# Kernel optimization log

Hardware: AMD Instinct MI355X
Metric: run time of the kernel (lower is better)

## Reference

```python
import jax, jax.numpy as jnp
import numpy as np

B, S, H, NH, HD = 2, 2048, 1024, 16, 64
RD = 16            # rotary_dim = head_dim * 0.25
W = 16             # mini_context_length (sliding window)
SCALE = HD ** -0.5
ROPE_BASE = 10000.0


def setup_inputs() -> dict:
    key = jax.random.key(0)
    ks = jax.random.split(key, 10)
    p = lambda k, shape: (jax.random.normal(k, shape, dtype=jnp.float32) * 0.02)
    return {
        "hidden_states": jax.random.normal(ks[0], (B, S, H), dtype=jnp.float32),
        "Wqkv": p(ks[1], (3 * H, H)), "bqkv": p(ks[2], (3 * H,)),
        "Wqa": p(ks[3], (H, H)),      "bqa": p(ks[4], (H,)),
        "Wka": p(ks[5], (H, H)),      "bka": p(ks[6], (H,)),
        "Wd": p(ks[7], (H, H)),       "bd": p(ks[8], (H,)),
    }


def _rotate_half(x):
    x1, x2 = jnp.split(x, 2, axis=-1)
    return jnp.concatenate([-x2, x1], axis=-1)


def _apply_rope(q, k, seq_len):
    # GPT-NeoX style rotary on the first RD dims. q,k: [B,NH,S,RD]
    inv_freq = 1.0 / (ROPE_BASE ** (jnp.arange(0, RD, 2, dtype=jnp.float32) / RD))
    t = jnp.arange(seq_len, dtype=jnp.float32)
    freqs = jnp.outer(t, inv_freq)                     # [S, RD//2]
    emb = jnp.concatenate([freqs, freqs], axis=-1)     # [S, RD]
    cos = jnp.cos(emb)[None, None]                      # [1,1,S,RD]
    sin = jnp.sin(emb)[None, None]
    return q * cos + _rotate_half(q) * sin, k * cos + _rotate_half(k) * sin


def reference(hidden_states, Wqkv, bqkv, Wqa, bqa, Wka, bka, Wd, bd):
    b, s, _ = hidden_states.shape
    qkv = hidden_states @ Wqkv.T + bqkv                       # [B,S,3H]
    qkv = qkv.reshape(b, s, 3, NH, HD).transpose(2, 0, 3, 1, 4)
    q, k, v = qkv[0], qkv[1], qkv[2]                          # [B,NH,S,HD]

    q_rot, k_rot = _apply_rope(q[..., :RD], k[..., :RD], s)
    q = jnp.concatenate([q_rot, q[..., RD:]], axis=-1)
    k = jnp.concatenate([k_rot, k[..., RD:]], axis=-1)

    # ----- Stage 1: sliding-window local attention (vectorized) -----
    pos = jnp.arange(s)
    idx = pos[:, None] - (W - 1) + jnp.arange(W)[None, :]     # [S,W]
    valid = idx >= 0
    idxc = jnp.clip(idx, 0, s - 1)
    k_win = k[:, :, idxc, :]                                   # [B,NH,S,W,HD]
    v_win = v[:, :, idxc, :]
    scores = jnp.einsum('bhsd,bhswd->bhsw', q, k_win) * SCALE
    scores = jnp.where(valid[None, None], scores, -jnp.inf)
    probs = jax.nn.softmax(scores, axis=-1)
    A = jnp.einsum('bhsw,bhswd->bhsd', probs, v_win)           # [B,NH,S,HD]

    A_hidden = A.transpose(0, 2, 1, 3).reshape(b, s, H)        # [B,S,H]

    # ----- Stage 2: causal global attention over A -----
    qa = (A_hidden @ Wqa.T + bqa).reshape(b, s, NH, HD).transpose(0, 2, 1, 3)
    ka = (A_hidden @ Wka.T + bka).reshape(b, s, NH, HD).transpose(0, 2, 1, 3)
    g = jnp.einsum('bhqd,bhkd->bhqk', qa, ka) * SCALE          # [B,NH,S,S]
    causal = pos[:, None] >= pos[None, :]
    g = jnp.where(causal[None, None], g, -jnp.inf)
    pg = jax.nn.softmax(g, axis=-1)
    out = jnp.einsum('bhqk,bhkd->bhqd', pg, A)                 # [B,NH,S,HD]
    out = out.transpose(0, 2, 1, 3).reshape(b, s, H)
    return out @ Wd.T + bd
```

## Files before the change

### kernel.cpp

```cpp
#include <hip/hip_runtime.h>
#include <hip/hip_bf16.h>
#include <cstdint>
#include <cstddef>

typedef __bf16 bf16;
typedef __bf16 bf16x2 __attribute__((ext_vector_type(2)));
typedef __bf16 bf16x4 __attribute__((ext_vector_type(4)));
typedef __bf16 bf16x8 __attribute__((ext_vector_type(8)));
typedef float  f32x4  __attribute__((ext_vector_type(4)));
typedef int    i32x4  __attribute__((ext_vector_type(4)));

#define DEVINL __device__ __forceinline__

constexpr int   Bc  = 2, Sc = 2048, Hc = 1024, NHc = 16, HDc = 64;
constexpr int   Tc  = Bc * Sc;
constexpr float L2E = 1.44269504088896340736f;
constexpr float NEG_BIG = -1.0e30f;

typedef __attribute__((address_space(1))) void AS1void;
typedef __attribute__((address_space(3))) void AS3void;

DEVINL void load_lds16(const bf16* g, bf16* l) {
  __builtin_amdgcn_global_load_lds((AS1void*)g, (AS3void*)l, 16, 0, 0);
}

DEVINL int packbf(float a, float b) {
  union { bf16x2 h; int i; } u;
  u.h[0] = (bf16)a; u.h[1] = (bf16)b;
  return u.i;
}


__global__ __launch_bounds__(256)
void convert_all(const float* __restrict__ hs, const float* __restrict__ Wqkv,
                 const float* __restrict__ Wqa, const float* __restrict__ Wka,
                 const float* __restrict__ Wd, const float* __restrict__ bqa,
                 const float* __restrict__ bka,
                 bf16* __restrict__ hsb, bf16* __restrict__ wqkvb,
                 bf16* __restrict__ wqakab, bf16* __restrict__ wdb,
                 float* __restrict__ bqaka) {
  const int blk = blockIdx.x;
  if (blk >= 5120) {
    const int i = threadIdx.x * 8;
    const float* src = (i < 1024) ? (bqa + i) : (bka + i - 1024);
    *(f32x4*)(bqaka + i)     = *(const f32x4*)src;
    *(f32x4*)(bqaka + i + 4) = *(const f32x4*)(src + 4);
    return;
  }
  const float* src; bf16* dst; int base;
  if      (blk < 2048) { src = hs;   dst = hsb;                    base = blk; }
  else if (blk < 3584) { src = Wqkv; dst = wqkvb;                  base = blk - 2048; }
  else if (blk < 4096) { src = Wqa;  dst = wqakab;                 base = blk - 3584; }
  else if (blk < 4608) { src = Wka;  dst = wqakab + 1024 * 1024;   base = blk - 4096; }
  else                 { src = Wd;   dst = wdb;                    base = blk - 4608; }
  const int i = (base * 256 + threadIdx.x) * 8;
  f32x4 a = *(const f32x4*)(src + i);
  f32x4 b = *(const f32x4*)(src + i + 4);
  bf16x8 v;
#pragma unroll
  for (int j = 0; j < 4; j++) { v[j] = (bf16)a[j]; v[4 + j] = (bf16)b[j]; }
  *(bf16x8*)(dst + i) = v;
}

template <typename CT>
__global__ __launch_bounds__(256, 3)
void gemm128(const bf16* __restrict__ A, const bf16* __restrict__ Bw,
             const float* __restrict__ bias, CT* __restrict__ C,
             int M, int N, int K) {
  __shared__ __attribute__((aligned(16))) bf16 As[128 * 64];
  __shared__ __attribute__((aligned(16))) bf16 Bs[128 * 64];

  const int tid = threadIdx.x, wv = tid >> 6, lane = tid & 63;
  const int m0 = blockIdx.y * 128, n0 = blockIdx.x * 128;
  const int col = lane & 15, quad = lane >> 4;
  const int wrow = (wv >> 1) * 64, wcol = (wv & 1) * 64;

  f32x4 acc[4][4];
#pragma unroll
  for (int i = 0; i < 4; i++)
#pragma unroll
    for (int j = 0; j < 4; j++) acc[i][j] = f32x4{0.f, 0.f, 0.f, 0.f};

  const int srow = tid >> 3;
  const int scol = (((tid & 7) ^ (srow & 7)) << 3);
  const bf16* Ag = A  + (size_t)(m0 + srow) * K + scol;
  const bf16* Bg = Bw + (size_t)(n0 + srow) * K + scol;
  const int cs = col & 7;

  for (int k0 = 0; k0 < K; k0 += 64) {
#pragma unroll
    for (int c = 0; c < 4; c++) {
      load_lds16(Ag + (size_t)(c * 32) * K + k0, As + c * 2048 + tid * 8);
      load_lds16(Bg + (size_t)(c * 32) * K + k0, Bs + c * 2048 + tid * 8);
    }
    __syncthreads();
#pragma unroll
    for (int kk = 0; kk < 64; kk += 32) {
      const int so = ((((kk >> 3) + quad) ^ cs) << 3);
      bf16x8 af[4], bfr[4];
#pragma unroll
      for (int i = 0; i < 4; i++)
        af[i] = *(const bf16x8*)(As + (wrow + i * 16 + col) * 64 + so);
#pragma unroll
      for (int j = 0; j < 4; j++)
        bfr[j] = *(const bf16x8*)(Bs + (wcol + j * 16 + col) * 64 + so);
#pragma unroll
      for (int i = 0; i < 4; i++)
#pragma unroll
        for (int j = 0; j < 4; j++)
          acc[i][j] = __builtin_amdgcn_mfma_f32_16x16x32_bf16(af[i], bfr[j], acc[i][j], 0, 0, 0);
    }
    __syncthreads();
  }

#pragma unroll
  for (int j = 0; j < 4; j++) {
    const int c = n0 + wcol + j * 16 + col;
    const float bv = bias[c];
#pragma unroll
    for (int i = 0; i < 4; i++)
#pragma unroll
      for (int r = 0; r < 4; r++) {
        const int rr = m0 + wrow + i * 16 + quad * 4 + r;
        C[(size_t)rr * N + c] = (CT)(acc[i][j][r] + bv);
      }
  }
}

template <typename CT>
__global__ __launch_bounds__(256, 4)
void gemm6464(const bf16* __restrict__ A, const bf16* __restrict__ Bw,
              const float* __restrict__ bias, CT* __restrict__ C,
              int M, int N, int K) {
  __shared__ __attribute__((aligned(16))) bf16 As[64 * 64];
  __shared__ __attribute__((aligned(16))) bf16 Bs[64 * 64];

  const int tid = threadIdx.x, wv = tid >> 6, lane = tid & 63;
  const int m0 = blockIdx.y * 64, n0 = blockIdx.x * 64;
  const int col = lane & 15, quad = lane >> 4;

  f32x4 acc[4];
#pragma unroll
  for (int j = 0; j < 4; j++) acc[j] = f32x4{0.f, 0.f, 0.f, 0.f};

  const int srow = tid >> 3;
  const int scol = (((tid & 7) ^ (srow & 7)) << 3);
  const bf16* Ag = A  + (size_t)(m0 + srow) * K + scol;
  const bf16* Bg = Bw + (size_t)(n0 + srow) * K + scol;
  const int cs = col & 7;

  for (int k0 = 0; k0 < K; k0 += 64) {
#pragma unroll
    for (int c = 0; c < 2; c++) {
      load_lds16(Ag + (size_t)(c * 32) * K + k0, As + c * 2048 + tid * 8);
      load_lds16(Bg + (size_t)(c * 32) * K + k0, Bs + c * 2048 + tid * 8);
    }
    __syncthreads();
#pragma unroll
    for (int kk = 0; kk < 64; kk += 32) {
      const int so = ((((kk >> 3) + quad) ^ cs) << 3);
      bf16x8 af = *(const bf16x8*)(As + (wv * 16 + col) * 64 + so);
#pragma unroll
      for (int j = 0; j < 4; j++) {
        bf16x8 bfr = *(const bf16x8*)(Bs + (j * 16 + col) * 64 + so);
        acc[j] = __builtin_amdgcn_mfma_f32_16x16x32_bf16(af, bfr, acc[j], 0, 0, 0);
      }
    }
    __syncthreads();
  }

#pragma unroll
  for (int j = 0; j < 4; j++) {
    const int c = n0 + j * 16 + col;
    const float bv = bias[c];
#pragma unroll
    for (int r = 0; r < 4; r++) {
      const int rr = m0 + wv * 16 + quad * 4 + r;
      C[(size_t)rr * N + c] = (CT)(acc[j][r] + bv);
    }
  }
}

__global__ __launch_bounds__(256)
void window_attn(const bf16* __restrict__ qkv, bf16* __restrict__ Ah,
                 bf16* __restrict__ VTg) {
  __shared__ __attribute__((aligned(16))) bf16 Kw[31 * 72];
  __shared__ __attribute__((aligned(16))) bf16 Vw[31 * 72];
  const int g  = blockIdx.x;
  const int st = g & 127;
  const int h  = (g >> 7) & 15;
  const int b  = g >> 11;
  const int s0 = st * 16;
  const int tid = threadIdx.x;

  if ((tid < 124) || (tid >= 128 && tid < 252)) {
    const bool isK = tid < 124;
    const int lt  = isK ? tid : tid - 128;
    const int r   = lt >> 2, off = (lt & 3) << 4;
    int sidx = s0 - 15 + r; if (sidx < 0) sidx = 0;
    const bf16* src = qkv + (size_t)(b * Sc + sidx) * 3072 + (isK ? 1024 : 2048) + h * 64 + off;
    bf16x8 v0 = *(const bf16x8*)src;
    bf16x8 v1 = *(const bf16x8*)(src + 8);
    if (isK && off == 0) {
#pragma unroll
      for (int j = 0; j < 8; j++) {
        const float invf = exp2f(-(float)j * 1.66096404744368128f);
        float sn, csn;
        sincosf((float)sidx * invf, &sn, &csn);
        const float x1 = (float)v0[j], x2 = (float)v1[j];
        v0[j] = (bf16)(x1 * csn - x2 * sn);
        v1[j] = (bf16)(x2 * csn + x1 * sn);
      }
    }
    bf16* dst = (isK ? Kw : Vw) + r * 72 + off;
    *(bf16x8*)dst       = v0;
    *(bf16x8*)(dst + 8) = v1;
  }
  __syncthreads();

  const int wv = tid >> 6, lane = tid & 63;
  const int subq = lane >> 4, lane16 = lane & 15;
  const int s = s0 + wv * 4 + subq;
  const int t = b * Sc + s;
  const int d0 = lane16 * 4;

  float qd[4];
  {
    bf16x4 qv = *(const bf16x4*)(qkv + (size_t)t * 3072 + h * 64 + d0);
#pragma unroll
    for (int j = 0; j < 4; j++) qd[j] = (float)qv[j];
  }
  float pd[4];
#pragma unroll
  for (int j = 0; j < 4; j++) pd[j] = __shfl_xor(qd[j], 2, 64);
  if (lane16 < 4) {
#pragma unroll
    for (int j = 0; j < 4; j++) {
      const int jabs = d0 + j;
      const float invf = exp2f(-(float)(jabs & 7) * 1.66096404744368128f);
      float sn, csn;
      sincosf((float)s * invf, &sn, &csn);
      qd[j] = (jabs < 8) ? (qd[j] * csn - pd[j] * sn) : (qd[j] * csn + pd[j] * sn);
    }
  }

  float sc[16];
#pragma unroll
  for (int w = 0; w < 16; w++) {
    const int idxp = s - 15 + w;
    const int row = idxp - s0 + 15;
    bf16x4 kv = *(const bf16x4*)(Kw + row * 72 + d0);
    float p = qd[0] * (float)kv[0] + qd[1] * (float)kv[1] +
              qd[2] * (float)kv[2] + qd[3] * (float)kv[3];
#pragma unroll
    for (int m = 1; m < 16; m <<= 1) p += __shfl_xor(p, m, 64);
    sc[w] = (idxp < 0) ? NEG_BIG : p * 0.125f;
  }
  float mx = sc[0];
#pragma unroll
  for (int w = 1; w < 16; w++) mx = fmaxf(mx, sc[w]);
  float sum = 0.f;
#pragma unroll
  for (int w = 0; w < 16; w++) { sc[w] = exp2f((sc[w] - mx) * L2E); sum += sc[w]; }
  const float inv = 1.0f / fmaxf(sum, 1e-30f);

  float acc[4] = {0.f, 0.f, 0.f, 0.f};
#pragma unroll
  for (int w = 0; w < 16; w++) {
    const int idxp = s - 15 + w;
    const int row = idxp - s0 + 15;
    bf16x4 vv = *(const bf16x4*)(Vw + row * 72 + d0);
#pragma unroll
    for (int j = 0; j < 4; j++) acc[j] += sc[w] * (float)vv[j];
  }
  bf16x4 ov;
#pragma unroll
  for (int j = 0; j < 4; j++) ov[j] = (bf16)(acc[j] * inv);
  *(bf16x4*)(Ah + (size_t)t * 1024 + h * 64 + d0) = ov;
  bf16* vt = VTg + (((size_t)(b * 16 + h)) * 64 + d0) * 2048 + s;
#pragma unroll
  for (int j = 0; j < 4; j++) vt[(size_t)j * 2048] = ov[j];
}

__global__ __launch_bounds__(256, 4)
void flash_attn(const bf16* __restrict__ Q, const bf16* __restrict__ Kt,
                const bf16* __restrict__ VTg, bf16* __restrict__ O) {
  constexpr int QS = 2048;
  constexpr float SHIFT = 16.0f;
  __shared__ __attribute__((aligned(16))) bf16 K_lds[128 * 64];
  __shared__ __attribute__((aligned(16))) bf16 VT_lds[64 * 128];

  const int tid = threadIdx.x, wv = tid >> 6, lane = tid & 63;
  const int bh = blockIdx.x;
  const int y  = blockIdx.y;
  const int gq = y & 7, kq = y >> 3;
  const int qt = (kq == 0) ? gq : (kq == 1) ? (15 - gq)
               : (kq == 2) ? (16 + gq) : (31 - gq);
  const int b = bh >> 4, h = bh & 15;
  const int col = lane & 15, quad = lane >> 4;
  const size_t bS = (size_t)b * Sc;
  const int hd = h * 64;

  const int krow = tid >> 3;
  const int kcol = (((tid & 7) ^ (krow & 7)) << 3);
  const int vrow = tid >> 4;
  const int vcol = (((tid & 15) ^ vrow) << 3);
  const int cs8 = col & 7;

  const int idxA = (col + 16 * ((2 * quad) & 3)) << 2;
  const int idxB = (col + 16 * ((2 * quad + 1) & 3)) << 2;

  const int qbase = qt * 64 + wv * 16;
  const int nkt = (qt + 2) >> 1;

  const bf16* qptr = Q + (bS + qbase + col) * QS + hd + quad * 8;
  bf16x8 qf[2];
  qf[0] = *(const bf16x8*)qptr;
  qf[1] = *(const bf16x8*)(qptr + 32);
#pragma unroll
  for (int hh = 0; hh < 2; hh++)
#pragma unroll
    for (int j = 0; j < 8; j++) qf[hh][j] = (bf16)((float)qf[hh][j] * 0.125f);

  f32x4 oacc[4];
#pragma unroll
  for (int i = 0; i < 4; i++) oacc[i] = f32x4{0.f, 0.f, 0.f, 0.f};
  float lsum = 0.f;

  for (int kt0 = 0; kt0 < nkt; kt0++) {
    const int k0 = kt0 * 128;
#pragma unroll
    for (int c = 0; c < 4; c++) {
      load_lds16(Kt + (bS + k0 + c * 32 + krow) * QS + hd + kcol,
                 K_lds + c * 2048 + tid * 8);
      load_lds16(VTg + ((size_t)bh * 64 + c * 16 + vrow) * 2048 + k0 + vcol,
                 VT_lds + c * 2048 + tid * 8);
    }
    __syncthreads();

    f32x4 sacc[8];
#pragma unroll
    for (int sub = 0; sub < 8; sub++) {
      f32x4 a = f32x4{0.f, 0.f, 0.f, 0.f};
#pragma unroll
      for (int hh = 0; hh < 2; hh++) {
        const int so = (((hh * 4 + quad) ^ cs8) << 3);
        bf16x8 kf = *(const bf16x8*)(K_lds + (sub * 16 + col) * 64 + so);
        a = __builtin_amdgcn_mfma_f32_16x16x32_bf16(kf, qf[hh], a, 0, 0, 0);
      }
      sacc[sub] = a;
    }
    if (kt0 == nkt - 1) {
      const int qq = qbase + col;
#pragma unroll
      for (int sub = 0; sub < 8; sub++)
#pragma unroll
        for (int r = 0; r < 4; r++) {
          const int key = k0 + sub * 16 + quad * 4 + r;
          if (key > qq) sacc[sub][r] = NEG_BIG;
        }
    }
#pragma unroll
    for (int sub = 0; sub < 8; sub++)
#pragma unroll
      for (int r = 0; r < 4; r++)
        sacc[sub][r] = exp2f(sacc[sub][r] * L2E - SHIFT);
#pragma unroll
    for (int sub = 0; sub < 8; sub++)
      lsum += (sacc[sub][0] + sacc[sub][1]) + (sacc[sub][2] + sacc[sub][3]);
    int pkl[8], pkh[8];
#pragma unroll
    for (int sub = 0; sub < 8; sub++) {
      pkl[sub] = packbf(sacc[sub][0], sacc[sub][1]);
      pkh[sub] = packbf(sacc[sub][2], sacc[sub][3]);
    }
#pragma unroll
    for (int c = 0; c < 4; c++) {
      const int sLo = 2 * c, sHi = 2 * c + 1;
      i32x4 w;
      {
        int aL = __builtin_amdgcn_ds_bpermute(idxA, pkl[sLo]);
        int aH = __builtin_amdgcn_ds_bpermute(idxA, pkl[sHi]);
        w[0] = (quad < 2) ? aL : aH;
      }
      {
        int aL = __builtin_amdgcn_ds_bpermute(idxA, pkh[sLo]);
        int aH = __builtin_amdgcn_ds_bpermute(idxA, pkh[sHi]);
        w[1] = (quad < 2) ? aL : aH;
      }
      {
        int aL = __builtin_amdgcn_ds_bpermute(idxB, pkl[sLo]);
        int aH = __builtin_amdgcn_ds_bpermute(idxB, pkl[sHi]);
        w[2] = (quad < 2) ? aL : aH;
      }
      {
        int aL = __builtin_amdgcn_ds_bpermute(idxB, pkh[sLo]);
        int aH = __builtin_amdgcn_ds_bpermute(idxB, pkh[sHi]);
        w[3] = (quad < 2) ? aL : aH;
      }
      union { i32x4 wi; bf16x8 v; } pb;
      pb.wi = w;
      const int vso = (((c * 4 + quad) ^ col) << 3);
#pragma unroll
      for (int nb = 0; nb < 4; nb++) {
        bf16x8 vf = *(const bf16x8*)(VT_lds + (nb * 16 + col) * 128 + vso);
        oacc[nb] = __builtin_amdgcn_mfma_f32_16x16x32_bf16(vf, pb.v, oacc[nb], 0, 0, 0);
      }
    }
    __syncthreads();
  }

  lsum += __shfl_xor(lsum, 16, 64);
  lsum += __shfl_xor(lsum, 32, 64);
  const float inv = 1.0f / fmaxf(lsum, 1e-37f);
  const int qq = qbase + col;
#pragma unroll
  for (int nb = 0; nb < 4; nb++) {
    bf16x4 ov;
#pragma unroll
    for (int r = 0; r < 4; r++) ov[r] = (bf16)(oacc[nb][r] * inv);
    *(bf16x4*)(O + (bS + qq) * 1024 + hd + nb * 16 + quad * 4) = ov;
  }
}

extern "C" void kernel_launch(void* const* d_in, const int* in_sizes, int n_in,
                              void* d_out, int out_size, void* d_ws, size_t ws_size,
                              hipStream_t stream) {
  (void)in_sizes; (void)n_in; (void)out_size; (void)ws_size;
  const float* hs   = (const float*)d_in[0];
  const float* Wqkv = (const float*)d_in[1];
  const float* bqkv = (const float*)d_in[2];
  const float* Wqa  = (const float*)d_in[3];
  const float* bqa  = (const float*)d_in[4];
  const float* Wka  = (const float*)d_in[5];
  const float* bka  = (const float*)d_in[6];
  const float* Wd   = (const float*)d_in[7];
  const float* bd   = (const float*)d_in[8];
  float* out = (float*)d_out;

  const size_t TH = (size_t)Tc * Hc;
  bf16* dob   = (bf16*)d_out;
  bf16* hsb   = dob;
  bf16* wqkvb = dob + TH;
  bf16* Ah    = dob;
  bf16* VTg   = dob + TH;
  bf16* ws     = (bf16*)d_ws;
  bf16* qkv    = ws;
  bf16* qaka   = ws;
  bf16* oh     = ws + 2 * TH;
  bf16* wqakab = ws + 3 * TH;
  bf16* wdb    = wqakab + 2 * 1024 * 1024;
  float* bqaka = (float*)(wdb + 1024 * 1024);

  convert_all<<<dim3(5121), 256, 0, stream>>>(hs, Wqkv, Wqa, Wka, Wd, bqa, bka,
                                              hsb, wqkvb, wqakab, wdb, bqaka);

  gemm128<bf16><<<dim3(24, 32), 256, 0, stream>>>(hsb, wqkvb, bqkv, qkv, Tc, 3 * Hc, Hc);
  window_attn<<<dim3(Tc * NHc / 16), 256, 0, stream>>>(qkv, Ah, VTg);
  gemm128<bf16><<<dim3(16, 32), 256, 0, stream>>>(Ah, wqakab, bqaka, qaka, Tc, 2 * Hc, Hc);
  flash_attn<<<dim3(Bc * NHc, 32), 256, 0, stream>>>(qaka, qaka + Hc, VTg, oh);
  gemm6464<float><<<dim3(16, 64), 256, 0, stream>>>(oh, wdb, bd, out, Tc, Hc, Hc);
}
```

Baseline: 240.8 us.

## Fuse fp32 weight conversion into GEMM B-tile staging

Drops the separate weight-conversion pass. The GEMMs now read fp32 weights directly and convert them to bf16 while staging tiles into LDS, and the Q/K projection weights and biases are selected per row through a split pointer instead of being pre-concatenated. This removes one pass that writes about 12 MB of converted weights and the buffers that held them. In exchange, the B operand is loaded through registers instead of the async global-to-LDS path, at twice the bytes per tile and re-read by every M block, which may slow the GEMM main loops.

```diff
diff --git a/kernel.cpp b/kernel.cpp
--- a/kernel.cpp
+++ b/kernel.cpp
@@ -24,6 +24,16 @@
   __builtin_amdgcn_global_load_lds((AS1void*)g, (AS3void*)l, 16, 0, 0);
 }
 
+DEVINL void stage8(const bf16* g, bf16* l) { load_lds16(g, l); }
+DEVINL void stage8(const float* g, bf16* l) {
+  f32x4 a = *(const f32x4*)g;
+  f32x4 b = *(const f32x4*)(g + 4);
+  bf16x8 v;
+#pragma unroll
+  for (int j = 0; j < 4; j++) { v[j] = (bf16)a[j]; v[4 + j] = (bf16)b[j]; }
+  *(bf16x8*)l = v;
+}
+
 DEVINL int packbf(float a, float b) {
   union { bf16x2 h; int i; } u;
   u.h[0] = (bf16)a; u.h[1] = (bf16)b;
@@ -32,40 +42,21 @@
 
 
 __global__ __launch_bounds__(256)
-void convert_all(const float* __restrict__ hs, const float* __restrict__ Wqkv,
-                 const float* __restrict__ Wqa, const float* __restrict__ Wka,
-                 const float* __restrict__ Wd, const float* __restrict__ bqa,
-                 const float* __restrict__ bka,
-                 bf16* __restrict__ hsb, bf16* __restrict__ wqkvb,
-                 bf16* __restrict__ wqakab, bf16* __restrict__ wdb,
-                 float* __restrict__ bqaka) {
-  const int blk = blockIdx.x;
-  if (blk >= 5120) {
-    const int i = threadIdx.x * 8;
-    const float* src = (i < 1024) ? (bqa + i) : (bka + i - 1024);
-    *(f32x4*)(bqaka + i)     = *(const f32x4*)src;
-    *(f32x4*)(bqaka + i + 4) = *(const f32x4*)(src + 4);
-    return;
-  }
-  const float* src; bf16* dst; int base;
-  if      (blk < 2048) { src = hs;   dst = hsb;                    base = blk; }
-  else if (blk < 3584) { src = Wqkv; dst = wqkvb;                  base = blk - 2048; }
-  else if (blk < 4096) { src = Wqa;  dst = wqakab;                 base = blk - 3584; }
-  else if (blk < 4608) { src = Wka;  dst = wqakab + 1024 * 1024;   base = blk - 4096; }
-  else                 { src = Wd;   dst = wdb;                    base = blk - 4608; }
-  const int i = (base * 256 + threadIdx.x) * 8;
-  f32x4 a = *(const f32x4*)(src + i);
-  f32x4 b = *(const f32x4*)(src + i + 4);
+void convert_hs(const float* __restrict__ in, bf16* __restrict__ out) {
+  const int i = (blockIdx.x * 256 + threadIdx.x) * 8;
+  f32x4 a = *(const f32x4*)(in + i);
+  f32x4 b = *(const f32x4*)(in + i + 4);
   bf16x8 v;
 #pragma unroll
   for (int j = 0; j < 4; j++) { v[j] = (bf16)a[j]; v[4 + j] = (bf16)b[j]; }
-  *(bf16x8*)(dst + i) = v;
-}
-
-template <typename CT>
+  *(bf16x8*)(out + i) = v;
+}
+
+template <typename BT, typename CT>
 __global__ __launch_bounds__(256, 3)
-void gemm128(const bf16* __restrict__ A, const bf16* __restrict__ Bw,
-             const float* __restrict__ bias, CT* __restrict__ C,
+void gemm128(const bf16* __restrict__ A, const BT* __restrict__ B1,
+             const BT* __restrict__ B2, const float* __restrict__ bias1,
+             const float* __restrict__ bias2, int nsplit, CT* __restrict__ C,
              int M, int N, int K) {
   __shared__ __attribute__((aligned(16))) bf16 As[128 * 64];
   __shared__ __attribute__((aligned(16))) bf16 Bs[128 * 64];
@@ -83,15 +74,21 @@
 
   const int srow = tid >> 3;
   const int scol = (((tid & 7) ^ (srow & 7)) << 3);
-  const bf16* Ag = A  + (size_t)(m0 + srow) * K + scol;
-  const bf16* Bg = Bw + (size_t)(n0 + srow) * K + scol;
+  const bf16* Ag = A + (size_t)(m0 + srow) * K + scol;
+  const BT* Bg[4];
+#pragma unroll
+  for (int c = 0; c < 4; c++) {
+    const int brow = n0 + c * 32 + srow;
+    Bg[c] = (brow < nsplit) ? B1 + (size_t)brow * K + scol
+                            : B2 + (size_t)(brow - nsplit) * K + scol;
+  }
   const int cs = col & 7;
 
   for (int k0 = 0; k0 < K; k0 += 64) {
 #pragma unroll
     for (int c = 0; c < 4; c++) {
       load_lds16(Ag + (size_t)(c * 32) * K + k0, As + c * 2048 + tid * 8);
-      load_lds16(Bg + (size_t)(c * 32) * K + k0, Bs + c * 2048 + tid * 8);
+      stage8(Bg[c] + k0, Bs + c * 2048 + tid * 8);
     }
     __syncthreads();
 #pragma unroll
@@ -116,7 +113,7 @@
 #pragma unroll
   for (int j = 0; j < 4; j++) {
     const int c = n0 + wcol + j * 16 + col;
-    const float bv = bias[c];
+    const float bv = (c < nsplit) ? bias1[c] : bias2[c - nsplit];
 #pragma unroll
     for (int i = 0; i < 4; i++)
 #pragma unroll
@@ -127,9 +124,9 @@
   }
 }
 
-template <typename CT>
+template <typename BT, typename CT>
 __global__ __launch_bounds__(256, 4)
-void gemm6464(const bf16* __restrict__ A, const bf16* __restrict__ Bw,
+void gemm6464(const bf16* __restrict__ A, const BT* __restrict__ Bw,
               const float* __restrict__ bias, CT* __restrict__ C,
               int M, int N, int K) {
   __shared__ __attribute__((aligned(16))) bf16 As[64 * 64];
@@ -146,14 +143,14 @@
   const int srow = tid >> 3;
   const int scol = (((tid & 7) ^ (srow & 7)) << 3);
   const bf16* Ag = A  + (size_t)(m0 + srow) * K + scol;
-  const bf16* Bg = Bw + (size_t)(n0 + srow) * K + scol;
+  const BT*   Bg = Bw + (size_t)(n0 + srow) * K + scol;
   const int cs = col & 7;
 
   for (int k0 = 0; k0 < K; k0 += 64) {
 #pragma unroll
     for (int c = 0; c < 2; c++) {
       load_lds16(Ag + (size_t)(c * 32) * K + k0, As + c * 2048 + tid * 8);
-      load_lds16(Bg + (size_t)(c * 32) * K + k0, Bs + c * 2048 + tid * 8);
+      stage8(Bg + (size_t)(c * 32) * K + k0, Bs + c * 2048 + tid * 8);
     }
     __syncthreads();
 #pragma unroll
@@ -439,25 +436,23 @@
   float* out = (float*)d_out;
 
   const size_t TH = (size_t)Tc * Hc;
-  bf16* dob   = (bf16*)d_out;
-  bf16* hsb   = dob;
-  bf16* wqkvb = dob + TH;
-  bf16* Ah    = dob;
-  bf16* VTg   = dob + TH;
-  bf16* ws     = (bf16*)d_ws;
-  bf16* qkv    = ws;
-  bf16* qaka   = ws;
-  bf16* oh     = ws + 2 * TH;
-  bf16* wqakab = ws + 3 * TH;
-  bf16* wdb    = wqakab + 2 * 1024 * 1024;
-  float* bqaka = (float*)(wdb + 1024 * 1024);
-
-  convert_all<<<dim3(5121), 256, 0, stream>>>(hs, Wqkv, Wqa, Wka, Wd, bqa, bka,
-                                              hsb, wqkvb, wqakab, wdb, bqaka);
-
-  gemm128<bf16><<<dim3(24, 32), 256, 0, stream>>>(hsb, wqkvb, bqkv, qkv, Tc, 3 * Hc, Hc);
+  bf16* dob = (bf16*)d_out;
+  bf16* hsb = dob;
+  bf16* Ah  = dob;
+  bf16* VTg = dob + TH;
+  bf16* ws   = (bf16*)d_ws;
+  bf16* qkv  = ws;
+  bf16* qaka = ws;
+  bf16* oh   = ws + 2 * TH;
+
+  convert_hs<<<dim3(2048), 256, 0, stream>>>(hs, hsb);
+
+  gemm128<float, bf16><<<dim3(24, 32), 256, 0, stream>>>(
+      hsb, Wqkv, Wqkv, bqkv, bqkv, 3 * Hc, qkv, Tc, 3 * Hc, Hc);
   window_attn<<<dim3(Tc * NHc / 16), 256, 0, stream>>>(qkv, Ah, VTg);
-  gemm128<bf16><<<dim3(16, 32), 256, 0, stream>>>(Ah, wqakab, bqaka, qaka, Tc, 2 * Hc, Hc);
+  gemm128<float, bf16><<<dim3(16, 32), 256, 0, stream>>>(
+      Ah, Wqa, Wka, bqa, bka, Hc, qaka, Tc, 2 * Hc, Hc);
   flash_attn<<<dim3(Bc * NHc, 32), 256, 0, stream>>>(qaka, qaka + Hc, VTg, oh);
-  gemm6464<float><<<dim3(16, 64), 256, 0, stream>>>(oh, wdb, bd, out, Tc, Hc, Hc);
-}
+  gemm6464<float, float><<<dim3(16, 64), 256, 0, stream>>>(
+      oh, Wd, bd, out, Tc, Hc, Hc);
+}
```

After: 249.0 us. +3.4%, slower.
